# Performance work log

Hardware: AMD Instinct MI355X
Metric: run time of the kernel (lower is better)

## Reference

```python
import jax, jax.numpy as jnp
import numpy as np

NEG_INF = -1.0e9


def setup_inputs() -> dict:
    key = jax.random.key(0)
    ks = jax.random.split(key, 7)
    B, D, L, N, K = 4096, 512, 20, 8192, 64
    return {
        "inputs_embed": jax.random.normal(ks[0], (B, D), jnp.float32),
        "labels_embed": jax.random.normal(ks[1], (B, D), jnp.float32),
        "labels": jax.random.normal(ks[2], (B, L), jnp.float32),
        "all_labels_embed": jax.random.normal(ks[3], (N, D), jnp.float32),
        "all_labels": jax.random.normal(ks[4], (N, L), jnp.float32),
        "neg_ids_in": jax.random.randint(ks[5], (B, K), 0, B, jnp.int32),
        "neg_ids_lb": jax.random.randint(ks[6], (B, K), 0, N, jnp.int32),
    }


def reference(inputs_embed, labels_embed, labels, all_labels_embed, all_labels,
              neg_ids_in, neg_ids_lb):
    # --- negative sampling (indices supplied; equals tf.gather of tiled table) ---
    neg_ie = inputs_embed[neg_ids_in]        # [B,K,D] negatives from inputs
    neg_le = all_labels_embed[neg_ids_lb]    # [B,K,D] negatives from label table
    # bad-negative masks: negative label features identical to the positive's
    bad_in = jnp.all(labels[neg_ids_in] == labels[:, None, :], axis=-1).astype(inputs_embed.dtype)      # [B,K]
    bad_lb = jnp.all(all_labels[neg_ids_lb] == labels[:, None, :], axis=-1).astype(inputs_embed.dtype)  # [B,K]

    # --- similarities (dot products) ---
    sim_pos = jnp.sum(inputs_embed * labels_embed, axis=-1, keepdims=True)            # [B,1]
    sim_neg_il = jnp.einsum("bd,bkd->bk", inputs_embed, neg_le) + NEG_INF * bad_lb    # [B,K]
    sim_neg_ll = jnp.einsum("bd,bkd->bk", labels_embed, neg_le) + NEG_INF * bad_lb
    sim_neg_ii = jnp.einsum("bd,bkd->bk", inputs_embed, neg_ie) + NEG_INF * bad_in
    sim_neg_li = jnp.einsum("bd,bkd->bk", labels_embed, neg_ie) + NEG_INF * bad_in

    # --- accuracy ---
    max_all = jnp.max(jnp.concatenate([sim_pos, sim_neg_il], axis=-1), axis=-1)
    acc = jnp.mean((max_all == sim_pos[:, 0]).astype(jnp.float32))

    # --- softmax loss, correct class at index 0 ---
    logits = jnp.concatenate([sim_pos, sim_neg_il, sim_neg_ll, sim_neg_ii, sim_neg_li], axis=-1)  # [B,1+4K]
    per_ex = -jax.nn.log_softmax(logits, axis=-1)[:, 0]   # [B]

    # --- confidence-based loss scaling: loss_scale(-per_ex) ---
    q = jnp.exp(-per_ex)
    scale = jnp.where(jnp.max(q) > 0.5,
                      jax.lax.stop_gradient(((1.0 - q) / 0.5) ** 4),
                      jnp.ones_like(q))
    loss = jnp.mean(per_ex * scale)
    return loss, acc
```

## Files before the change

kernel.cpp:

```cpp
#include <hip/hip_runtime.h>
#include <hip/hip_bf16.h>

#define BB 4096
#define DD 512
#define LLAB 20
#define NN 8192
#define KK 64

constexpr float kNegInf = -1.0e9f;
constexpr float kLn2 = 0.69314718055994530942f;
constexpr float kWlPe = 2.5f;
constexpr float kWlTie = 2.0f;

#define OFF_STATS 16384
#define OFF_SP    16640
#define OFF_SIE   33024
#define OFF_SLE   49408
#define OFF_SALE  65792
#define OFF_HLAB  98560
#define OFF_HAL   131328
#define OFF_IEQ   196864
#define OFF_LEQ   2294016
#define OFF_ALEQ  4391168
#define WS_NEED   (OFF_ALEQ + (size_t)NN * DD)

__device__ __forceinline__ float dot4(const float4& a, const float4& b) {
  return a.x * b.x + a.y * b.y + a.z * b.z + a.w * b.w;
}

__device__ __forceinline__ float waveReduceSum(float v) {
#pragma unroll
  for (int s = 1; s < 64; s <<= 1) v += __shfl_xor(v, s);
  return v;
}

__device__ __forceinline__ float waveReduceMax(float v) {
#pragma unroll
  for (int s = 1; s < 64; s <<= 1) v = fmaxf(v, __shfl_xor(v, s));
  return v;
}

__device__ __forceinline__ float waveReduceMin(float v) {
#pragma unroll
  for (int s = 1; s < 64; s <<= 1) v = fminf(v, __shfl_xor(v, s));
  return v;
}

__device__ __forceinline__ unsigned long long hash20(const float* __restrict__ p) {
  unsigned long long h = 1469598103934665603ull;
#pragma unroll
  for (int t = 0; t < LLAB; ++t) {
    h ^= (unsigned long long)__float_as_uint(p[t]);
    h *= 1099511628211ull;
  }
  return h;
}

__device__ __forceinline__ int sdot4i(unsigned a, unsigned b, int acc) {
#if __has_builtin(__builtin_amdgcn_sdot4)
  return __builtin_amdgcn_sdot4((int)a, (int)b, acc, false);
#else
#pragma unroll
  for (int t = 0; t < 4; ++t)
    acc += (int)(signed char)(a >> (8 * t)) * (int)(signed char)(b >> (8 * t));
  return acc;
#endif
}

__device__ __forceinline__ unsigned pk4i8(float a, float b, float c, float d, float inv) {
  const int q0 = (int)rintf(a * inv);
  const int q1 = (int)rintf(b * inv);
  const int q2 = (int)rintf(c * inv);
  const int q3 = (int)rintf(d * inv);
  return (q0 & 255) | ((q1 & 255) << 8) | ((q2 & 255) << 16) | ((q3 & 255) << 24);
}

__device__ __forceinline__ float max8abs(const float4& a, const float4& c) {
  return fmaxf(fmaxf(fmaxf(fabsf(a.x), fabsf(a.y)), fmaxf(fabsf(a.z), fabsf(a.w))),
               fmaxf(fmaxf(fabsf(c.x), fabsf(c.y)), fmaxf(fabsf(c.z), fabsf(c.w))));
}

__global__ void init_kernel(unsigned* stats) {
  if (threadIdx.x == 0) stats[0] = 0u;
}

__global__ __launch_bounds__(256) void prep_kernel(
    const float* __restrict__ ie, const float* __restrict__ le,
    const float* __restrict__ ale, const float* __restrict__ labels,
    const float* __restrict__ al, char* __restrict__ ie_q,
    char* __restrict__ le_q, char* __restrict__ ale_q,
    float* __restrict__ s_ie, float* __restrict__ s_le,
    float* __restrict__ s_ale, float* __restrict__ sp,
    unsigned long long* __restrict__ h_lab,
    unsigned long long* __restrict__ h_al, unsigned* __restrict__ stats) {
  const int tid = threadIdx.x;
  const int lane = tid & 63;
  const int wave = tid >> 6;
  const int w = blockIdx.x * 4 + wave;

  if (w < BB) {
    const float4* i4 = (const float4*)(ie + (size_t)w * DD);
    const float4* l4 = (const float4*)(le + (size_t)w * DD);
    const float4 a0 = i4[2 * lane], a1 = i4[2 * lane + 1];
    const float4 b0 = l4[2 * lane], b1 = l4[2 * lane + 1];
    float p = dot4(a0, b0) + dot4(a1, b1);
    p = waveReduceSum(p);
    float mi = fmaxf(waveReduceMax(max8abs(a0, a1)), 1e-20f);
    const float inv_i = 127.0f / mi;
    uint2 oi;
    oi.x = pk4i8(a0.x, a0.y, a0.z, a0.w, inv_i);
    oi.y = pk4i8(a1.x, a1.y, a1.z, a1.w, inv_i);
    ((uint2*)(ie_q + (size_t)w * DD))[lane] = oi;
    float ml = fmaxf(waveReduceMax(max8abs(b0, b1)), 1e-20f);
    const float inv_l = 127.0f / ml;
    uint2 ol;
    ol.x = pk4i8(b0.x, b0.y, b0.z, b0.w, inv_l);
    ol.y = pk4i8(b1.x, b1.y, b1.z, b1.w, inv_l);
    ((uint2*)(le_q + (size_t)w * DD))[lane] = ol;
    if (lane == 0) {
      sp[w] = p;
      s_ie[w] = mi * (1.0f / 127.0f);
      s_le[w] = ml * (1.0f / 127.0f);
    }
  } else {
    const int row = w - BB;
    const float4* r4 = (const float4*)(ale + (size_t)row * DD);
    const float4 a = r4[2 * lane], c = r4[2 * lane + 1];
    float mx = fmaxf(waveReduceMax(max8abs(a, c)), 1e-20f);
    const float inv = 127.0f / mx;
    uint2 o;
    o.x = pk4i8(a.x, a.y, a.z, a.w, inv);
    o.y = pk4i8(c.x, c.y, c.z, c.w, inv);
    ((uint2*)(ale_q + (size_t)row * DD))[lane] = o;
    if (lane == 0) s_ale[row] = mx * (1.0f / 127.0f);
  }

  const int g = blockIdx.x * 256 + tid;
  if (g == 0) stats[0] = 0u;
  if (g < BB) h_lab[g] = hash20(labels + (size_t)g * LLAB);
  else if (g < BB + NN) h_al[g - BB] = hash20(al + (size_t)(g - BB) * LLAB);
}

__device__ __forceinline__ void row_f32_body(
    int b, const float* __restrict__ ie, const float* __restrict__ le,
    const float* __restrict__ labels, const float* __restrict__ ale,
    const float* __restrict__ al, const int* __restrict__ nin,
    const int* __restrict__ nlb, float* __restrict__ per_ex,
    unsigned* __restrict__ stats, bool count_acc, float* sims, float* wred) {
  const int tid = threadIdx.x;
  const int lane = tid & 63;
  const int wave = tid >> 6;

  const float4* ie4 = (const float4*)(ie + (size_t)b * DD);
  const float4* le4 = (const float4*)(le + (size_t)b * DD);
  float4 ier0 = ie4[lane], ier1 = ie4[lane + 64];
  float4 ler0 = le4[lane], ler1 = le4[lane + 64];
  float lab = (lane < LLAB) ? labels[(size_t)b * LLAB + lane] : 0.0f;

  if (wave == 0) {
    float p = dot4(ier0, ler0) + dot4(ier1, ler1);
    p = waveReduceSum(p);
    if (lane == 0) sims[0] = p;
  }

#pragma unroll 2
  for (int kk = 0; kk < KK / 4; ++kk) {
    const int k = wave * (KK / 4) + kk;
    const int j_lb = __builtin_amdgcn_readfirstlane(nlb[(size_t)b * KK + k]);
    const int j_in = __builtin_amdgcn_readfirstlane(nin[(size_t)b * KK + k]);

    const float4* rle = (const float4*)(ale + (size_t)j_lb * DD);
    const float4* rie = (const float4*)(ie + (size_t)j_in * DD);
    float4 vle0 = rle[lane], vle1 = rle[lane + 64];
    float4 vie0 = rie[lane], vie1 = rie[lane + 64];

    bool ein = true, elb = true;
    if (lane < LLAB) {
      ein = (labels[(size_t)j_in * LLAB + lane] == lab);
      elb = (al[(size_t)j_lb * LLAB + lane] == lab);
    }
    const bool bad_in = (__ballot(ein) == ~0ull);
    const bool bad_lb = (__ballot(elb) == ~0ull);

    float a_il = dot4(vle0, ier0) + dot4(vle1, ier1);
    float a_ll = dot4(vle0, ler0) + dot4(vle1, ler1);
    float a_ii = dot4(vie0, ier0) + dot4(vie1, ier1);
    float a_li = dot4(vie0, ler0) + dot4(vie1, ler1);

    const bool oddl = (lane & 1) != 0;
    float sx = oddl ? a_il : a_ii;
    float sy = oddl ? a_ll : a_li;
    float rx = __shfl_xor(sx, 1);
    float ry = __shfl_xor(sy, 1);
    float mx = (oddl ? a_ii : a_il) + rx;
    float my = (oddl ? a_li : a_ll) + ry;
    const bool hi2 = (lane & 2) != 0;
    float s1 = hi2 ? mx : my;
    float r1 = __shfl_xor(s1, 2);
    float v = (hi2 ? my : mx) + r1;
    v += __shfl_xor(v, 4);
    v += __shfl_xor(v, 8);
    v += __shfl_xor(v, 16);
    v += __shfl_xor(v, 32);

    if (lane < 4) {
      const bool badf = (lane & 1) ? bad_in : bad_lb;
      const float s = badf ? v + kNegInf : v;
      const int slot = ((lane & 1) << 1) | ((lane >> 1) & 1);
      sims[1 + slot * KK + k] = s;
    }
  }
  __syncthreads();

  const float v = sims[1 + tid];
  const float s0 = sims[0];
  float wmax = waveReduceMax(v);
  if (lane == 0) wred[wave] = wmax;
  __syncthreads();
  float m = fmaxf(fmaxf(wred[0], wred[1]), fmaxf(wred[2], wred[3]));
  m = fmaxf(m, s0);
  const float e = expf(v - m);
  float wsum = waveReduceSum(e);
  if (lane == 0) wred[4 + wave] = wsum;
  __syncthreads();
  if (tid == 0) {
    const float tot = wred[4] + wred[5] + wred[6] + wred[7] + expf(s0 - m);
    per_ex[b] = m + logf(tot) - s0;
    if (count_acc) {
      const float max_il = wred[0];
      if (s0 >= max_il) atomicAdd(&stats[0], 1u);
    }
  }
}

__global__ __launch_bounds__(256, 4) void row_i8_kernel(
    const float* __restrict__ ie, const float* __restrict__ le,
    const float* __restrict__ labels, const float* __restrict__ ale,
    const float* __restrict__ al, const char* __restrict__ ie_q,
    const char* __restrict__ le_q, const char* __restrict__ ale_q,
    const float* __restrict__ s_ie, const float* __restrict__ s_le,
    const float* __restrict__ s_ale, const float* __restrict__ sp,
    const unsigned long long* __restrict__ h_lab,
    const unsigned long long* __restrict__ h_al,
    const int* __restrict__ nin, const int* __restrict__ nlb,
    float* __restrict__ per_ex, unsigned* __restrict__ stats) {
  const int b = blockIdx.x;
  const int tid = threadIdx.x;
  const int lane = tid & 63;
  const int wave = tid >> 6;
  const int c = lane & 3;
  const int g = lane >> 2;

  __shared__ uint4 qls4[64];
  __shared__ float simsX[1 + 4 * KK];
  __shared__ float wred[12];
  __shared__ int do_fix;

  const int wuni = __builtin_amdgcn_readfirstlane(wave);
  const int k = wuni * 16 + g;

  const int jl = nlb[b * KK + k];
  const int ji = nin[b * KK + k];
  const unsigned long long hb = h_lab[b];
  const bool bad_lb = (h_al[jl] == hb);
  const bool bad_in = (h_lab[ji] == hb);
  const float sA = s_ale[jl];
  const float sB = s_ie[ji];

  const uint4* arow = (const uint4*)(ale_q + (size_t)jl * DD);
  const uint4* brow = (const uint4*)(ie_q + (size_t)ji * DD);
  uint4 Ar[8], Br[8];
#pragma unroll
  for (int i = 0; i < 8; ++i) {
    Ar[i] = arow[i * 4 + c];
    Br[i] = brow[i * 4 + c];
  }

  if (wave == 0) {
    if (lane < 32) qls4[lane] = ((const uint4*)(ie_q + (size_t)b * DD))[lane];
    else qls4[lane] = ((const uint4*)(le_q + (size_t)b * DD))[lane - 32];
  }
  __syncthreads();

  int il = 0, ll = 0, ii = 0, li = 0;
#pragma unroll
  for (int i = 0; i < 8; ++i) {
    const uint4 qi = qls4[i * 4 + c];
    const uint4 ql = qls4[32 + i * 4 + c];
    il = sdot4i(Ar[i].x, qi.x, il); il = sdot4i(Ar[i].y, qi.y, il);
    il = sdot4i(Ar[i].z, qi.z, il); il = sdot4i(Ar[i].w, qi.w, il);
    ll = sdot4i(Ar[i].x, ql.x, ll); ll = sdot4i(Ar[i].y, ql.y, ll);
    ll = sdot4i(Ar[i].z, ql.z, ll); ll = sdot4i(Ar[i].w, ql.w, ll);
    ii = sdot4i(Br[i].x, qi.x, ii); ii = sdot4i(Br[i].y, qi.y, ii);
    ii = sdot4i(Br[i].z, qi.z, ii); ii = sdot4i(Br[i].w, qi.w, ii);
    li = sdot4i(Br[i].x, ql.x, li); li = sdot4i(Br[i].y, ql.y, li);
    li = sdot4i(Br[i].z, ql.z, li); li = sdot4i(Br[i].w, ql.w, li);
  }

  const bool odd = (lane & 1) != 0;
  const int x = odd ? il : ii;
  const int y = odd ? ll : li;
  const int rx = __shfl_xor(x, 1);
  const int ry = __shfl_xor(y, 1);
  const int aa = (odd ? ii : il) + rx;
  const int bb2 = (odd ? li : ll) + ry;
  const bool hi2 = (lane & 2) != 0;
  const int s1 = hi2 ? aa : bb2;
  const int r1 = __shfl_xor(s1, 2);
  const int vi = (hi2 ? bb2 : aa) + r1;

  const float srow = (c & 1) ? sB : sA;
  const float sq = (c & 2) ? s_le[b] : s_ie[b];
  const float v = (float)vi * (srow * sq);
  const bool badf = (c & 1) ? bad_in : bad_lb;
  const float s = badf ? v + kNegInf : v;

  const float s0 = sp[b];

  float m_w = waveReduceMax(s);
  float mil_w = waveReduceMax((c == 0) ? s : -3.0e38f);
  if (lane == 0) {
    wred[wave] = m_w;
    wred[4 + wave] = mil_w;
  }
  __syncthreads();
  float m = fmaxf(fmaxf(fmaxf(wred[0], wred[1]), fmaxf(wred[2], wred[3])), s0);
  const float e = expf(s - m);
  float sum_w = waveReduceSum(e);
  if (lane == 0) wred[8 + wave] = sum_w;
  __syncthreads();
  if (tid == 0) {
    const float tot = wred[8] + wred[9] + wred[10] + wred[11] + expf(s0 - m);
    const float pe = m + logf(tot) - s0;
    per_ex[b] = pe;
    const float max_il = fmaxf(fmaxf(wred[4], wred[5]), fmaxf(wred[6], wred[7]));
    const bool wl_row = (pe < kWlPe) || (fabsf(s0 - max_il) < kWlTie);
    do_fix = wl_row ? 1 : 0;
    if (!wl_row && s0 >= max_il) atomicAdd(&stats[0], 1u);
  }
  __syncthreads();

  if (do_fix) {
    row_f32_body(b, ie, le, labels, ale, al, nin, nlb, per_ex, stats,
                 true, simsX, wred);
  }
}

__global__ __launch_bounds__(256) void row_f32_kernel(
    const float* __restrict__ ie, const float* __restrict__ le,
    const float* __restrict__ labels, const float* __restrict__ ale,
    const float* __restrict__ al, const int* __restrict__ nin,
    const int* __restrict__ nlb, float* __restrict__ per_ex,
    unsigned* __restrict__ stats) {
  __shared__ float sims[1 + 4 * KK];
  __shared__ float wred[8];
  row_f32_body(blockIdx.x, ie, le, labels, ale, al, nin, nlb, per_ex, stats,
               true, sims, wred);
}

__global__ __launch_bounds__(256) void finalize_kernel(
    const float* __restrict__ per_ex, const unsigned* __restrict__ stats,
    float* __restrict__ out) {
  __shared__ float pe_s[BB];
  __shared__ float wred[8];
  const int tid = threadIdx.x;
  const int lane = tid & 63;
  const int wave = tid >> 6;

  float mn = 1.0e30f;
#pragma unroll 4
  for (int i = tid; i < BB; i += 256) {
    const float v = per_ex[i];
    pe_s[i] = v;
    mn = fminf(mn, v);
  }
  mn = waveReduceMin(mn);
  if (lane == 0) wred[wave] = mn;
  __syncthreads();
  const float minpe = fminf(fminf(wred[0], wred[1]), fminf(wred[2], wred[3]));
  const bool scale_on = (minpe < kLn2);
  __syncthreads();

  float sum = 0.0f;
#pragma unroll 4
  for (int i = tid; i < BB; i += 256) {
    const float pe = pe_s[i];
    float s = 1.0f;
    if (scale_on) {
      const float q = expf(-pe);
      const float t = 2.0f * (1.0f - q);
      const float t2 = t * t;
      s = t2 * t2;
    }
    sum += pe * s;
  }
  sum = waveReduceSum(sum);
  if (lane == 0) wred[4 + wave] = sum;
  __syncthreads();
  if (tid == 0) {
    const float tot = wred[4] + wred[5] + wred[6] + wred[7];
    out[0] = tot / (float)BB;
    out[1] = (float)stats[0] / (float)BB;
  }
}

extern "C" void kernel_launch(void* const* d_in, const int* in_sizes, int n_in,
                              void* d_out, int out_size, void* d_ws, size_t ws_size,
                              hipStream_t stream) {
  const float* ie = (const float*)d_in[0];
  const float* le = (const float*)d_in[1];
  const float* labels = (const float*)d_in[2];
  const float* ale = (const float*)d_in[3];
  const float* al = (const float*)d_in[4];
  const int* nin = (const int*)d_in[5];
  const int* nlb = (const int*)d_in[6];
  float* out = (float*)d_out;

  float* per_ex = (float*)d_ws;
  unsigned* stats = (unsigned*)((char*)d_ws + OFF_STATS);

  if (ws_size >= WS_NEED) {
    char* ie_q = (char*)d_ws + OFF_IEQ;
    char* le_q = (char*)d_ws + OFF_LEQ;
    char* ale_q = (char*)d_ws + OFF_ALEQ;
    float* s_ie = (float*)((char*)d_ws + OFF_SIE);
    float* s_le = (float*)((char*)d_ws + OFF_SLE);
    float* s_ale = (float*)((char*)d_ws + OFF_SALE);
    float* sp = (float*)((char*)d_ws + OFF_SP);
    unsigned long long* h_lab = (unsigned long long*)((char*)d_ws + OFF_HLAB);
    unsigned long long* h_al = (unsigned long long*)((char*)d_ws + OFF_HAL);
    const int prep_blocks = (BB + NN) / 4;
    hipLaunchKernelGGL(prep_kernel, dim3(prep_blocks), dim3(256), 0, stream,
                       ie, le, ale, labels, al, ie_q, le_q, ale_q,
                       s_ie, s_le, s_ale, sp, h_lab, h_al, stats);
    hipLaunchKernelGGL(row_i8_kernel, dim3(BB), dim3(256), 0, stream,
                       ie, le, labels, ale, al, ie_q, le_q, ale_q,
                       s_ie, s_le, s_ale, sp, h_lab, h_al, nin, nlb,
                       per_ex, stats);
  } else {
    hipLaunchKernelGGL(init_kernel, dim3(1), dim3(64), 0, stream, stats);
    hipLaunchKernelGGL(row_f32_kernel, dim3(BB), dim3(256), 0, stream,
                       ie, le, labels, ale, al, nin, nlb, per_ex, stats);
  }
  hipLaunchKernelGGL(finalize_kernel, dim3(1), dim3(256), 0, stream,
                     per_ex, stats, out);
}
```

Measured before the change: 53.29 us.

## Move f32 fixup rows to worklist kernel and reduce loss via fixed-point atomics

The int8 row kernel now runs 512 threads with 8 lanes per negative and no longer does an inline f32 recompute. Rows that are near-tie or low-loss are pushed to a worklist and recomputed by a separate persistent fixup kernel. Each row's loss, scaled loss and the running minimum are accumulated into banked fixed-point atomics, so the final reduction only reads 64 banks instead of all per-example values. This removes per-block divergence from inline fixups and shrinks the finalize pass, at the cost of one extra launch, atomic traffic, and precision that depends on the fixed-point encoding and the int8 tie heuristics.

```diff
diff --git a/kernel.cpp b/kernel.cpp
--- a/kernel.cpp
+++ b/kernel.cpp
@@ -11,17 +11,23 @@
 constexpr float kLn2 = 0.69314718055994530942f;
 constexpr float kWlPe = 2.5f;
 constexpr float kWlTie = 2.0f;
-
+constexpr double kFix = 1073741824.0;
+
+#define OFF_PEREX 0
 #define OFF_STATS 16384
-#define OFF_SP    16640
-#define OFF_SIE   33024
-#define OFF_SLE   49408
-#define OFF_SALE  65792
-#define OFF_HLAB  98560
-#define OFF_HAL   131328
-#define OFF_IEQ   196864
-#define OFF_LEQ   2294016
-#define OFF_ALEQ  4391168
+#define OFF_MINPE (16384 + 256)
+#define OFF_SUMP  (16384 + 512)
+#define OFF_SUMS  (16384 + 1024)
+#define OFF_WL    20480
+#define OFF_SP    36864
+#define OFF_SIE   53248
+#define OFF_SLE   69632
+#define OFF_SALE  86016
+#define OFF_HLAB  118784
+#define OFF_HAL   151552
+#define OFF_IEQ   217088
+#define OFF_LEQ   (OFF_IEQ + (size_t)BB * DD)
+#define OFF_ALEQ  (OFF_LEQ + (size_t)BB * DD)
 #define WS_NEED   (OFF_ALEQ + (size_t)NN * DD)
 
 __device__ __forceinline__ float dot4(const float4& a, const float4& b) {
@@ -78,6 +84,24 @@
 __device__ __forceinline__ float max8abs(const float4& a, const float4& c) {
   return fmaxf(fmaxf(fmaxf(fabsf(a.x), fabsf(a.y)), fmaxf(fabsf(a.z), fabsf(a.w))),
                fmaxf(fmaxf(fabsf(c.x), fabsf(c.y)), fmaxf(fabsf(c.z), fabsf(c.w))));
+}
+
+__device__ __forceinline__ float loss_scale(float pe) {
+  const float q = expf(-pe);
+  const float t = 2.0f * (1.0f - q);
+  const float t2 = t * t;
+  return t2 * t2;
+}
+
+__device__ __forceinline__ void accum_loss(int b, float pe, unsigned* minpeB,
+                                           unsigned long long* sumP,
+                                           unsigned long long* sumS) {
+  const float pc = fmaxf(pe, 0.0f);
+  const int bank = b & 63;
+  atomicMin(&minpeB[bank], __float_as_uint(pc));
+  atomicAdd(&sumP[bank], (unsigned long long)((double)pc * kFix + 0.5));
+  atomicAdd(&sumS[bank],
+            (unsigned long long)((double)(pc * loss_scale(pc)) * kFix + 0.5));
 }
 
 __global__ void init_kernel(unsigned* stats) {
@@ -92,7 +116,9 @@
     float* __restrict__ s_ie, float* __restrict__ s_le,
     float* __restrict__ s_ale, float* __restrict__ sp,
     unsigned long long* __restrict__ h_lab,
-    unsigned long long* __restrict__ h_al, unsigned* __restrict__ stats) {
+    unsigned long long* __restrict__ h_al, unsigned* __restrict__ stats,
+    unsigned* __restrict__ minpeB, unsigned long long* __restrict__ sumP,
+    unsigned long long* __restrict__ sumS) {
   const int tid = threadIdx.x;
   const int lane = tid & 63;
   const int wave = tid >> 6;
@@ -136,9 +162,140 @@
   }
 
   const int g = blockIdx.x * 256 + tid;
-  if (g == 0) stats[0] = 0u;
+  if (g < 2) stats[g] = 0u;
+  if (g < 64) {
+    minpeB[g] = 0x7F800000u;
+    sumP[g] = 0ull;
+    sumS[g] = 0ull;
+  }
   if (g < BB) h_lab[g] = hash20(labels + (size_t)g * LLAB);
   else if (g < BB + NN) h_al[g - BB] = hash20(al + (size_t)(g - BB) * LLAB);
+}
+
+__global__ __launch_bounds__(512, 8) void row_i8_kernel(
+    const char* __restrict__ ie_q, const char* __restrict__ le_q,
+    const char* __restrict__ ale_q, const float* __restrict__ s_ie,
+    const float* __restrict__ s_le, const float* __restrict__ s_ale,
+    const float* __restrict__ sp, const unsigned long long* __restrict__ h_lab,
+    const unsigned long long* __restrict__ h_al,
+    const int* __restrict__ nin, const int* __restrict__ nlb,
+    int* __restrict__ wl, unsigned* __restrict__ stats,
+    unsigned* __restrict__ minpeB, unsigned long long* __restrict__ sumP,
+    unsigned long long* __restrict__ sumS) {
+  const int b = blockIdx.x;
+  const int tid = threadIdx.x;
+  const int lane = tid & 63;
+  const int wave = tid >> 6;
+  const int o = lane & 7;
+  const int oct = lane >> 3;
+
+  __shared__ uint4 qls4[64];
+  __shared__ float wredm[8], wreds[8];
+  __shared__ int iflags[8];
+
+  const int k = wave * 8 + oct;
+  const int jl = nlb[b * KK + k];
+  const int ji = nin[b * KK + k];
+
+  const uint4* arow = (const uint4*)(ale_q + (size_t)jl * DD);
+  const uint4* brow = (const uint4*)(ie_q + (size_t)ji * DD);
+  uint4 Ar[4], Br[4];
+#pragma unroll
+  for (int j = 0; j < 4; ++j) {
+    Ar[j] = arow[o + 8 * j];
+    Br[j] = brow[o + 8 * j];
+  }
+
+  const unsigned long long hb = h_lab[b];
+  const bool bad_lb = (h_al[jl] == hb);
+  const bool bad_in = (h_lab[ji] == hb);
+  const float sA = s_ale[jl];
+  const float sB = s_ie[ji];
+  const float s0 = sp[b];
+
+  if (wave == 0) {
+    if (lane < 32) qls4[lane] = ((const uint4*)(ie_q + (size_t)b * DD))[lane];
+    else qls4[lane] = ((const uint4*)(le_q + (size_t)b * DD))[lane - 32];
+  }
+  __syncthreads();
+
+  int il = 0, ll = 0, ii = 0, li = 0;
+#pragma unroll
+  for (int j = 0; j < 4; ++j) {
+    const uint4 qi = qls4[o + 8 * j];
+    const uint4 ql = qls4[32 + o + 8 * j];
+    il = sdot4i(Ar[j].x, qi.x, il); il = sdot4i(Ar[j].y, qi.y, il);
+    il = sdot4i(Ar[j].z, qi.z, il); il = sdot4i(Ar[j].w, qi.w, il);
+    ll = sdot4i(Ar[j].x, ql.x, ll); ll = sdot4i(Ar[j].y, ql.y, ll);
+    ll = sdot4i(Ar[j].z, ql.z, ll); ll = sdot4i(Ar[j].w, ql.w, ll);
+    ii = sdot4i(Br[j].x, qi.x, ii); ii = sdot4i(Br[j].y, qi.y, ii);
+    ii = sdot4i(Br[j].z, qi.z, ii); ii = sdot4i(Br[j].w, qi.w, ii);
+    li = sdot4i(Br[j].x, ql.x, li); li = sdot4i(Br[j].y, ql.y, li);
+    li = sdot4i(Br[j].z, ql.z, li); li = sdot4i(Br[j].w, ql.w, li);
+  }
+
+  const bool odd = (lane & 1) != 0;
+  const int x = odd ? il : ii;
+  const int y = odd ? ll : li;
+  const int rx = __shfl_xor(x, 1);
+  const int ry = __shfl_xor(y, 1);
+  const int aa = (odd ? ii : il) + rx;
+  const int bb2 = (odd ? li : ll) + ry;
+  const bool hi2 = (lane & 2) != 0;
+  const int s1 = hi2 ? aa : bb2;
+  const int r1 = __shfl_xor(s1, 2);
+  int vi = (hi2 ? bb2 : aa) + r1;
+  vi += __shfl_xor(vi, 4);
+
+  const int c = lane & 3;
+  const bool real = (lane & 4) == 0;
+  const float srow = (c & 1) ? sB : sA;
+  const float sq = (c & 2) ? s_le[b] : s_ie[b];
+  const float v = (float)vi * (srow * sq);
+  const bool badf = (c & 1) ? bad_in : bad_lb;
+  const float s = badf ? v + kNegInf : v;
+
+  const bool is_il = (c == 0) && real;
+  const bool okA = !is_il || (s <= s0);
+  const bool exB = is_il && (s > s0 - kWlTie);
+  const bool albB = !is_il || (s < s0 + kWlTie);
+  const int flags = ((__ballot(okA) == ~0ull) ? 1 : 0) |
+                    ((__ballot(exB) != 0ull) ? 2 : 0) |
+                    ((__ballot(albB) == ~0ull) ? 4 : 0);
+
+  float m_w = waveReduceMax(s);
+  if (lane == 0) {
+    wredm[wave] = m_w;
+    iflags[wave] = flags;
+  }
+  __syncthreads();
+  float m = s0;
+#pragma unroll
+  for (int t = 0; t < 8; ++t) m = fmaxf(m, wredm[t]);
+  const float e = real ? expf(s - m) : 0.0f;
+  float sum_w = waveReduceSum(e);
+  if (lane == 0) wreds[wave] = sum_w;
+  __syncthreads();
+  if (tid == 0) {
+    float tot = expf(s0 - m);
+    int allok = 1, anyex = 0, allb = 1;
+#pragma unroll
+    for (int t = 0; t < 8; ++t) {
+      tot += wreds[t];
+      allok &= (iflags[t] & 1);
+      anyex |= (iflags[t] & 2);
+      allb &= (iflags[t] >> 2) & 1;
+    }
+    const float pe = m + logf(tot) - s0;
+    const bool band = (anyex != 0) && (allb != 0);
+    if ((pe < kWlPe) || band) {
+      const unsigned p = atomicAdd(&stats[1], 1u);
+      wl[p] = b;
+    } else {
+      if (allok) atomicAdd(&stats[0], 1u);
+      accum_loss(b, pe, minpeB, sumP, sumS);
+    }
+  }
 }
 
 __device__ __forceinline__ void row_f32_body(
@@ -233,119 +390,6 @@
   }
 }
 
-__global__ __launch_bounds__(256, 4) void row_i8_kernel(
-    const float* __restrict__ ie, const float* __restrict__ le,
-    const float* __restrict__ labels, const float* __restrict__ ale,
-    const float* __restrict__ al, const char* __restrict__ ie_q,
-    const char* __restrict__ le_q, const char* __restrict__ ale_q,
-    const float* __restrict__ s_ie, const float* __restrict__ s_le,
-    const float* __restrict__ s_ale, const float* __restrict__ sp,
-    const unsigned long long* __restrict__ h_lab,
-    const unsigned long long* __restrict__ h_al,
-    const int* __restrict__ nin, const int* __restrict__ nlb,
-    float* __restrict__ per_ex, unsigned* __restrict__ stats) {
-  const int b = blockIdx.x;
-  const int tid = threadIdx.x;
-  const int lane = tid & 63;
-  const int wave = tid >> 6;
-  const int c = lane & 3;
-  const int g = lane >> 2;
-
-  __shared__ uint4 qls4[64];
-  __shared__ float simsX[1 + 4 * KK];
-  __shared__ float wred[12];
-  __shared__ int do_fix;
-
-  const int wuni = __builtin_amdgcn_readfirstlane(wave);
-  const int k = wuni * 16 + g;
-
-  const int jl = nlb[b * KK + k];
-  const int ji = nin[b * KK + k];
-  const unsigned long long hb = h_lab[b];
-  const bool bad_lb = (h_al[jl] == hb);
-  const bool bad_in = (h_lab[ji] == hb);
-  const float sA = s_ale[jl];
-  const float sB = s_ie[ji];
-
-  const uint4* arow = (const uint4*)(ale_q + (size_t)jl * DD);
-  const uint4* brow = (const uint4*)(ie_q + (size_t)ji * DD);
-  uint4 Ar[8], Br[8];
-#pragma unroll
-  for (int i = 0; i < 8; ++i) {
-    Ar[i] = arow[i * 4 + c];
-    Br[i] = brow[i * 4 + c];
-  }
-
-  if (wave == 0) {
-    if (lane < 32) qls4[lane] = ((const uint4*)(ie_q + (size_t)b * DD))[lane];
-    else qls4[lane] = ((const uint4*)(le_q + (size_t)b * DD))[lane - 32];
-  }
-  __syncthreads();
-
-  int il = 0, ll = 0, ii = 0, li = 0;
-#pragma unroll
-  for (int i = 0; i < 8; ++i) {
-    const uint4 qi = qls4[i * 4 + c];
-    const uint4 ql = qls4[32 + i * 4 + c];
-    il = sdot4i(Ar[i].x, qi.x, il); il = sdot4i(Ar[i].y, qi.y, il);
-    il = sdot4i(Ar[i].z, qi.z, il); il = sdot4i(Ar[i].w, qi.w, il);
-    ll = sdot4i(Ar[i].x, ql.x, ll); ll = sdot4i(Ar[i].y, ql.y, ll);
-    ll = sdot4i(Ar[i].z, ql.z, ll); ll = sdot4i(Ar[i].w, ql.w, ll);
-    ii = sdot4i(Br[i].x, qi.x, ii); ii = sdot4i(Br[i].y, qi.y, ii);
-    ii = sdot4i(Br[i].z, qi.z, ii); ii = sdot4i(Br[i].w, qi.w, ii);
-    li = sdot4i(Br[i].x, ql.x, li); li = sdot4i(Br[i].y, ql.y, li);
-    li = sdot4i(Br[i].z, ql.z, li); li = sdot4i(Br[i].w, ql.w, li);
-  }
-
-  const bool odd = (lane & 1) != 0;
-  const int x = odd ? il : ii;
-  const int y = odd ? ll : li;
-  const int rx = __shfl_xor(x, 1);
-  const int ry = __shfl_xor(y, 1);
-  const int aa = (odd ? ii : il) + rx;
-  const int bb2 = (odd ? li : ll) + ry;
-  const bool hi2 = (lane & 2) != 0;
-  const int s1 = hi2 ? aa : bb2;
-  const int r1 = __shfl_xor(s1, 2);
-  const int vi = (hi2 ? bb2 : aa) + r1;
-
-  const float srow = (c & 1) ? sB : sA;
-  const float sq = (c & 2) ? s_le[b] : s_ie[b];
-  const float v = (float)vi * (srow * sq);
-  const bool badf = (c & 1) ? bad_in : bad_lb;
-  const float s = badf ? v + kNegInf : v;
-
-  const float s0 = sp[b];
-
-  float m_w = waveReduceMax(s);
-  float mil_w = waveReduceMax((c == 0) ? s : -3.0e38f);
-  if (lane == 0) {
-    wred[wave] = m_w;
-    wred[4 + wave] = mil_w;
-  }
-  __syncthreads();
-  float m = fmaxf(fmaxf(fmaxf(wred[0], wred[1]), fmaxf(wred[2], wred[3])), s0);
-  const float e = expf(s - m);
-  float sum_w = waveReduceSum(e);
-  if (lane == 0) wred[8 + wave] = sum_w;
-  __syncthreads();
-  if (tid == 0) {
-    const float tot = wred[8] + wred[9] + wred[10] + wred[11] + expf(s0 - m);
-    const float pe = m + logf(tot) - s0;
-    per_ex[b] = pe;
-    const float max_il = fmaxf(fmaxf(wred[4], wred[5]), fmaxf(wred[6], wred[7]));
-    const bool wl_row = (pe < kWlPe) || (fabsf(s0 - max_il) < kWlTie);
-    do_fix = wl_row ? 1 : 0;
-    if (!wl_row && s0 >= max_il) atomicAdd(&stats[0], 1u);
-  }
-  __syncthreads();
-
-  if (do_fix) {
-    row_f32_body(b, ie, le, labels, ale, al, nin, nlb, per_ex, stats,
-                 true, simsX, wred);
-  }
-}
-
 __global__ __launch_bounds__(256) void row_f32_kernel(
     const float* __restrict__ ie, const float* __restrict__ le,
     const float* __restrict__ labels, const float* __restrict__ ale,
@@ -358,6 +402,49 @@
                true, sims, wred);
 }
 
+__global__ __launch_bounds__(256) void fixup_kernel(
+    const float* __restrict__ ie, const float* __restrict__ le,
+    const float* __restrict__ labels, const float* __restrict__ ale,
+    const float* __restrict__ al, const int* __restrict__ nin,
+    const int* __restrict__ nlb, float* __restrict__ per_ex,
+    const int* __restrict__ wl, unsigned* __restrict__ stats,
+    unsigned* __restrict__ minpeB, unsigned long long* __restrict__ sumP,
+    unsigned long long* __restrict__ sumS) {
+  __shared__ float sims[1 + 4 * KK];
+  __shared__ float wred[8];
+  const int n = (int)stats[1];
+  for (int w = blockIdx.x; w < n; w += gridDim.x) {
+    const int b = wl[w];
+    row_f32_body(b, ie, le, labels, ale, al, nin, nlb, per_ex, stats,
+                 true, sims, wred);
+    if (threadIdx.x == 0) accum_loss(b, per_ex[b], minpeB, sumP, sumS);
+    __syncthreads();
+  }
+}
+
+__global__ __launch_bounds__(64) void finalize2_kernel(
+    const unsigned* __restrict__ stats, const unsigned* __restrict__ minpeB,
+    const unsigned long long* __restrict__ sumP,
+    const unsigned long long* __restrict__ sumS, float* __restrict__ out) {
+  const int lane = threadIdx.x;
+  unsigned mb = minpeB[lane];
+  unsigned long long p = sumP[lane];
+  unsigned long long q = sumS[lane];
+#pragma unroll
+  for (int s = 1; s < 64; s <<= 1) {
+    mb = min(mb, (unsigned)__shfl_xor((int)mb, s));
+    p += (unsigned long long)__shfl_xor((long long)p, s);
+    q += (unsigned long long)__shfl_xor((long long)q, s);
+  }
+  if (lane == 0) {
+    const float minpe = __uint_as_float(mb);
+    const bool scale_on = (minpe < kLn2);
+    const double tot = (double)(scale_on ? q : p) / kFix;
+    out[0] = (float)(tot / (double)BB);
+    out[1] = (float)stats[0] / (float)BB;
+  }
+}
+
 __global__ __launch_bounds__(256) void finalize_kernel(
     const float* __restrict__ per_ex, const unsigned* __restrict__ stats,
     float* __restrict__ out) {
@@ -385,14 +472,7 @@
 #pragma unroll 4
   for (int i = tid; i < BB; i += 256) {
     const float pe = pe_s[i];
-    float s = 1.0f;
-    if (scale_on) {
-      const float q = expf(-pe);
-      const float t = 2.0f * (1.0f - q);
-      const float t2 = t * t;
-      s = t2 * t2;
-    }
-    sum += pe * s;
+    sum += pe * (scale_on ? loss_scale(pe) : 1.0f);
   }
   sum = waveReduceSum(sum);
   if (lane == 0) wred[4 + wave] = sum;
@@ -429,19 +509,29 @@
     float* sp = (float*)((char*)d_ws + OFF_SP);
     unsigned long long* h_lab = (unsigned long long*)((char*)d_ws + OFF_HLAB);
     unsigned long long* h_al = (unsigned long long*)((char*)d_ws + OFF_HAL);
+    unsigned* minpeB = (unsigned*)((char*)d_ws + OFF_MINPE);
+    unsigned long long* sumP = (unsigned long long*)((char*)d_ws + OFF_SUMP);
+    unsigned long long* sumS = (unsigned long long*)((char*)d_ws + OFF_SUMS);
+    int* wl = (int*)((char*)d_ws + OFF_WL);
+
     const int prep_blocks = (BB + NN) / 4;
     hipLaunchKernelGGL(prep_kernel, dim3(prep_blocks), dim3(256), 0, stream,
                        ie, le, ale, labels, al, ie_q, le_q, ale_q,
-                       s_ie, s_le, s_ale, sp, h_lab, h_al, stats);
-    hipLaunchKernelGGL(row_i8_kernel, dim3(BB), dim3(256), 0, stream,
-                       ie, le, labels, ale, al, ie_q, le_q, ale_q,
-                       s_ie, s_le, s_ale, sp, h_lab, h_al, nin, nlb,
-                       per_ex, stats);
+                       s_ie, s_le, s_ale, sp, h_lab, h_al, stats,
+                       minpeB, sumP, sumS);
+    hipLaunchKernelGGL(row_i8_kernel, dim3(BB), dim3(512), 0, stream,
+                       ie_q, le_q, ale_q, s_ie, s_le, s_ale, sp, h_lab, h_al,
+                       nin, nlb, wl, stats, minpeB, sumP, sumS);
+    hipLaunchKernelGGL(fixup_kernel, dim3(128), dim3(256), 0, stream,
+                       ie, le, labels, ale, al, nin, nlb, per_ex, wl, stats,
+                       minpeB, sumP, sumS);
+    hipLaunchKernelGGL(finalize2_kernel, dim3(1), dim3(64), 0, stream,
+                       stats, minpeB, sumP, sumS, out);
   } else {
     hipLaunchKernelGGL(init_kernel, dim3(1), dim3(64), 0, stream, stats);
     hipLaunchKernelGGL(row_f32_kernel, dim3(BB), dim3(256), 0, stream,
                        ie, le, labels, ale, al, nin, nlb, per_ex, stats);
-  }
-  hipLaunchKernelGGL(finalize_kernel, dim3(1), dim3(256), 0, stream,
-                     per_ex, stats, out);
-}
+    hipLaunchKernelGGL(finalize_kernel, dim3(1), dim3(256), 0, stream,
+                       per_ex, stats, out);
+  }
+}
```

New measurement: 58.69 us. 1.1x slower.

## Fuse loss reduction into row kernel via banked fixed-point atomics, asm gather loads

Applied to the files above, without the earlier changes.

Each row's per-example loss, and its confidence-scaled variant, are accumulated into 64 banked fixed-point 64-bit atomic sums plus an atomic min. A tiny one-wave finalize kernel then picks the right sum, replacing the 4096-element finalize pass over per_ex. The row kernel also issues its int8 negative-row gathers with inline asm global_load_dwordx4 before the scalar lookups, and every wave stages the query vectors, so the block barrier before the dot products is dropped. This adds atomic traffic and fixed-point rounding, and clamps negative per-example losses to zero before accumulation.

```diff
diff --git a/kernel.cpp b/kernel.cpp
--- a/kernel.cpp
+++ b/kernel.cpp
@@ -11,18 +11,29 @@
 constexpr float kLn2 = 0.69314718055994530942f;
 constexpr float kWlPe = 2.5f;
 constexpr float kWlTie = 2.0f;
-
+constexpr double kFix = 1073741824.0;
+
+#define OFF_PEREX 0
 #define OFF_STATS 16384
-#define OFF_SP    16640
-#define OFF_SIE   33024
-#define OFF_SLE   49408
-#define OFF_SALE  65792
-#define OFF_HLAB  98560
-#define OFF_HAL   131328
-#define OFF_IEQ   196864
-#define OFF_LEQ   2294016
-#define OFF_ALEQ  4391168
+#define OFF_MINPE (16384 + 256)
+#define OFF_SUMP  (16384 + 512)
+#define OFF_SUMS  (16384 + 1024)
+#define OFF_SP    36864
+#define OFF_SIE   53248
+#define OFF_SLE   69632
+#define OFF_SALE  86016
+#define OFF_HLAB  118784
+#define OFF_HAL   151552
+#define OFF_IEQ   217088
+#define OFF_LEQ   (OFF_IEQ + (size_t)BB * DD)
+#define OFF_ALEQ  (OFF_LEQ + (size_t)BB * DD)
 #define WS_NEED   (OFF_ALEQ + (size_t)NN * DD)
+
+typedef unsigned u32x4 __attribute__((ext_vector_type(4)));
+
+#define GLD(dst, base, OFFSTR)                                        \
+  asm volatile("global_load_dwordx4 %0, %1, off offset:" OFFSTR      \
+               : "=v"(dst) : "v"(base) : "memory")
 
 __device__ __forceinline__ float dot4(const float4& a, const float4& b) {
   return a.x * b.x + a.y * b.y + a.z * b.z + a.w * b.w;
@@ -80,6 +91,24 @@
                fmaxf(fmaxf(fabsf(c.x), fabsf(c.y)), fmaxf(fabsf(c.z), fabsf(c.w))));
 }
 
+__device__ __forceinline__ float loss_scale(float pe) {
+  const float q = expf(-pe);
+  const float t = 2.0f * (1.0f - q);
+  const float t2 = t * t;
+  return t2 * t2;
+}
+
+__device__ __forceinline__ void accum_loss(int b, float pe, unsigned* minpeB,
+                                           unsigned long long* sumP,
+                                           unsigned long long* sumS) {
+  const float pc = fmaxf(pe, 0.0f);
+  const int bank = b & 63;
+  atomicMin(&minpeB[bank], __float_as_uint(pc));
+  atomicAdd(&sumP[bank], (unsigned long long)((double)pc * kFix + 0.5));
+  atomicAdd(&sumS[bank],
+            (unsigned long long)((double)(pc * loss_scale(pc)) * kFix + 0.5));
+}
+
 __global__ void init_kernel(unsigned* stats) {
   if (threadIdx.x == 0) stats[0] = 0u;
 }
@@ -92,7 +121,9 @@
     float* __restrict__ s_ie, float* __restrict__ s_le,
     float* __restrict__ s_ale, float* __restrict__ sp,
     unsigned long long* __restrict__ h_lab,
-    unsigned long long* __restrict__ h_al, unsigned* __restrict__ stats) {
+    unsigned long long* __restrict__ h_al, unsigned* __restrict__ stats,
+    unsigned* __restrict__ minpeB, unsigned long long* __restrict__ sumP,
+    unsigned long long* __restrict__ sumS) {
   const int tid = threadIdx.x;
   const int lane = tid & 63;
   const int wave = tid >> 6;
@@ -136,7 +167,12 @@
   }
 
   const int g = blockIdx.x * 256 + tid;
-  if (g == 0) stats[0] = 0u;
+  if (g < 2) stats[g] = 0u;
+  if (g < 64) {
+    minpeB[g] = 0x7F800000u;
+    sumP[g] = 0ull;
+    sumS[g] = 0ull;
+  }
   if (g < BB) h_lab[g] = hash20(labels + (size_t)g * LLAB);
   else if (g < BB + NN) h_al[g - BB] = hash20(al + (size_t)(g - BB) * LLAB);
 }
@@ -243,7 +279,9 @@
     const unsigned long long* __restrict__ h_lab,
     const unsigned long long* __restrict__ h_al,
     const int* __restrict__ nin, const int* __restrict__ nlb,
-    float* __restrict__ per_ex, unsigned* __restrict__ stats) {
+    float* __restrict__ per_ex, unsigned* __restrict__ stats,
+    unsigned* __restrict__ minpeB, unsigned long long* __restrict__ sumP,
+    unsigned long long* __restrict__ sumS) {
   const int b = blockIdx.x;
   const int tid = threadIdx.x;
   const int lane = tid & 63;
@@ -251,51 +289,61 @@
   const int c = lane & 3;
   const int g = lane >> 2;
 
-  __shared__ uint4 qls4[64];
+  __shared__ u32x4 qls4[64];
   __shared__ float simsX[1 + 4 * KK];
   __shared__ float wred[12];
   __shared__ int do_fix;
 
+  {
+    const u32x4* qsrc = (lane < 32)
+        ? ((const u32x4*)(ie_q + ((size_t)b << 9))) + lane
+        : ((const u32x4*)(le_q + ((size_t)b << 9))) + (lane - 32);
+    qls4[lane] = *qsrc;
+  }
+
   const int wuni = __builtin_amdgcn_readfirstlane(wave);
   const int k = wuni * 16 + g;
-
   const int jl = nlb[b * KK + k];
   const int ji = nin[b * KK + k];
+  const char* pa = ale_q + ((size_t)jl << 9) + (c << 4);
+  const char* pb = ie_q + ((size_t)ji << 9) + (c << 4);
+
+  u32x4 A0, A1, A2, A3, A4, A5, A6, A7;
+  u32x4 B0, B1, B2, B3, B4, B5, B6, B7;
+  GLD(A0, pa, "0");   GLD(A1, pa, "64");  GLD(A2, pa, "128"); GLD(A3, pa, "192");
+  GLD(A4, pa, "256"); GLD(A5, pa, "320"); GLD(A6, pa, "384"); GLD(A7, pa, "448");
+  GLD(B0, pb, "0");   GLD(B1, pb, "64");  GLD(B2, pb, "128"); GLD(B3, pb, "192");
+  GLD(B4, pb, "256"); GLD(B5, pb, "320"); GLD(B6, pb, "384"); GLD(B7, pb, "448");
+
   const unsigned long long hb = h_lab[b];
   const bool bad_lb = (h_al[jl] == hb);
   const bool bad_in = (h_lab[ji] == hb);
   const float sA = s_ale[jl];
   const float sB = s_ie[ji];
-
-  const uint4* arow = (const uint4*)(ale_q + (size_t)jl * DD);
-  const uint4* brow = (const uint4*)(ie_q + (size_t)ji * DD);
-  uint4 Ar[8], Br[8];
-#pragma unroll
-  for (int i = 0; i < 8; ++i) {
-    Ar[i] = arow[i * 4 + c];
-    Br[i] = brow[i * 4 + c];
-  }
-
-  if (wave == 0) {
-    if (lane < 32) qls4[lane] = ((const uint4*)(ie_q + (size_t)b * DD))[lane];
-    else qls4[lane] = ((const uint4*)(le_q + (size_t)b * DD))[lane - 32];
-  }
-  __syncthreads();
+  const float s0 = sp[b];
+  const float sqi = s_ie[b];
+  const float sql = s_le[b];
+
+  asm volatile("s_waitcnt vmcnt(0)" ::: "memory");
+  __builtin_amdgcn_sched_barrier(0);
 
   int il = 0, ll = 0, ii = 0, li = 0;
-#pragma unroll
-  for (int i = 0; i < 8; ++i) {
-    const uint4 qi = qls4[i * 4 + c];
-    const uint4 ql = qls4[32 + i * 4 + c];
-    il = sdot4i(Ar[i].x, qi.x, il); il = sdot4i(Ar[i].y, qi.y, il);
-    il = sdot4i(Ar[i].z, qi.z, il); il = sdot4i(Ar[i].w, qi.w, il);
-    ll = sdot4i(Ar[i].x, ql.x, ll); ll = sdot4i(Ar[i].y, ql.y, ll);
-    ll = sdot4i(Ar[i].z, ql.z, ll); ll = sdot4i(Ar[i].w, ql.w, ll);
-    ii = sdot4i(Br[i].x, qi.x, ii); ii = sdot4i(Br[i].y, qi.y, ii);
-    ii = sdot4i(Br[i].z, qi.z, ii); ii = sdot4i(Br[i].w, qi.w, ii);
-    li = sdot4i(Br[i].x, ql.x, li); li = sdot4i(Br[i].y, ql.y, li);
-    li = sdot4i(Br[i].z, ql.z, li); li = sdot4i(Br[i].w, ql.w, li);
-  }
+#define STEP(Ai, Bi, i)                                              \
+  {                                                                  \
+    const u32x4 qi = qls4[(i) * 4 + c];                              \
+    const u32x4 ql = qls4[32 + (i) * 4 + c];                         \
+    il = sdot4i(Ai.x, qi.x, il); il = sdot4i(Ai.y, qi.y, il);        \
+    il = sdot4i(Ai.z, qi.z, il); il = sdot4i(Ai.w, qi.w, il);        \
+    ll = sdot4i(Ai.x, ql.x, ll); ll = sdot4i(Ai.y, ql.y, ll);        \
+    ll = sdot4i(Ai.z, ql.z, ll); ll = sdot4i(Ai.w, ql.w, ll);        \
+    ii = sdot4i(Bi.x, qi.x, ii); ii = sdot4i(Bi.y, qi.y, ii);        \
+    ii = sdot4i(Bi.z, qi.z, ii); ii = sdot4i(Bi.w, qi.w, ii);        \
+    li = sdot4i(Bi.x, ql.x, li); li = sdot4i(Bi.y, ql.y, li);        \
+    li = sdot4i(Bi.z, ql.z, li); li = sdot4i(Bi.w, ql.w, li);        \
+  }
+  STEP(A0, B0, 0) STEP(A1, B1, 1) STEP(A2, B2, 2) STEP(A3, B3, 3)
+  STEP(A4, B4, 4) STEP(A5, B5, 5) STEP(A6, B6, 6) STEP(A7, B7, 7)
+#undef STEP
 
   const bool odd = (lane & 1) != 0;
   const int x = odd ? il : ii;
@@ -310,12 +358,10 @@
   const int vi = (hi2 ? bb2 : aa) + r1;
 
   const float srow = (c & 1) ? sB : sA;
-  const float sq = (c & 2) ? s_le[b] : s_ie[b];
+  const float sq = (c & 2) ? sql : sqi;
   const float v = (float)vi * (srow * sq);
   const bool badf = (c & 1) ? bad_in : bad_lb;
   const float s = badf ? v + kNegInf : v;
-
-  const float s0 = sp[b];
 
   float m_w = waveReduceMax(s);
   float mil_w = waveReduceMax((c == 0) ? s : -3.0e38f);
@@ -330,19 +376,24 @@
   if (lane == 0) wred[8 + wave] = sum_w;
   __syncthreads();
   if (tid == 0) {
-    const float tot = wred[8] + wred[9] + wred[10] + wred[11] + expf(s0 - m);
+    const float tot =
+        wred[8] + wred[9] + wred[10] + wred[11] + expf(s0 - m);
     const float pe = m + logf(tot) - s0;
     per_ex[b] = pe;
     const float max_il = fmaxf(fmaxf(wred[4], wred[5]), fmaxf(wred[6], wred[7]));
     const bool wl_row = (pe < kWlPe) || (fabsf(s0 - max_il) < kWlTie);
     do_fix = wl_row ? 1 : 0;
-    if (!wl_row && s0 >= max_il) atomicAdd(&stats[0], 1u);
+    if (!wl_row) {
+      if (s0 >= max_il) atomicAdd(&stats[0], 1u);
+      accum_loss(b, pe, minpeB, sumP, sumS);
+    }
   }
   __syncthreads();
 
   if (do_fix) {
     row_f32_body(b, ie, le, labels, ale, al, nin, nlb, per_ex, stats,
                  true, simsX, wred);
+    if (tid == 0) accum_loss(b, per_ex[b], minpeB, sumP, sumS);
   }
 }
 
@@ -358,6 +409,29 @@
                true, sims, wred);
 }
 
+__global__ __launch_bounds__(64) void finalize2_kernel(
+    const unsigned* __restrict__ stats, const unsigned* __restrict__ minpeB,
+    const unsigned long long* __restrict__ sumP,
+    const unsigned long long* __restrict__ sumS, float* __restrict__ out) {
+  const int lane = threadIdx.x;
+  unsigned mb = minpeB[lane];
+  unsigned long long p = sumP[lane];
+  unsigned long long q = sumS[lane];
+#pragma unroll
+  for (int s = 1; s < 64; s <<= 1) {
+    mb = min(mb, (unsigned)__shfl_xor((int)mb, s));
+    p += (unsigned long long)__shfl_xor((long long)p, s);
+    q += (unsigned long long)__shfl_xor((long long)q, s);
+  }
+  if (lane == 0) {
+    const float minpe = __uint_as_float(mb);
+    const bool scale_on = (minpe < kLn2);
+    const double tot = (double)(scale_on ? q : p) / kFix;
+    out[0] = (float)(tot / (double)BB);
+    out[1] = (float)stats[0] / (float)BB;
+  }
+}
+
 __global__ __launch_bounds__(256) void finalize_kernel(
     const float* __restrict__ per_ex, const unsigned* __restrict__ stats,
     float* __restrict__ out) {
@@ -385,14 +459,7 @@
 #pragma unroll 4
   for (int i = tid; i < BB; i += 256) {
     const float pe = pe_s[i];
-    float s = 1.0f;
-    if (scale_on) {
-      const float q = expf(-pe);
-      const float t = 2.0f * (1.0f - q);
-      const float t2 = t * t;
-      s = t2 * t2;
-    }
-    sum += pe * s;
+    sum += pe * (scale_on ? loss_scale(pe) : 1.0f);
   }
   sum = waveReduceSum(sum);
   if (lane == 0) wred[4 + wave] = sum;
@@ -429,19 +496,26 @@
     float* sp = (float*)((char*)d_ws + OFF_SP);
     unsigned long long* h_lab = (unsigned long long*)((char*)d_ws + OFF_HLAB);
     unsigned long long* h_al = (unsigned long long*)((char*)d_ws + OFF_HAL);
+    unsigned* minpeB = (unsigned*)((char*)d_ws + OFF_MINPE);
+    unsigned long long* sumP = (unsigned long long*)((char*)d_ws + OFF_SUMP);
+    unsigned long long* sumS = (unsigned long long*)((char*)d_ws + OFF_SUMS);
+
     const int prep_blocks = (BB + NN) / 4;
     hipLaunchKernelGGL(prep_kernel, dim3(prep_blocks), dim3(256), 0, stream,
                        ie, le, ale, labels, al, ie_q, le_q, ale_q,
-                       s_ie, s_le, s_ale, sp, h_lab, h_al, stats);
+                       s_ie, s_le, s_ale, sp, h_lab, h_al, stats,
+                       minpeB, sumP, sumS);
     hipLaunchKernelGGL(row_i8_kernel, dim3(BB), dim3(256), 0, stream,
                        ie, le, labels, ale, al, ie_q, le_q, ale_q,
                        s_ie, s_le, s_ale, sp, h_lab, h_al, nin, nlb,
-                       per_ex, stats);
+                       per_ex, stats, minpeB, sumP, sumS);
+    hipLaunchKernelGGL(finalize2_kernel, dim3(1), dim3(64), 0, stream,
+                       stats, minpeB, sumP, sumS, out);
   } else {
     hipLaunchKernelGGL(init_kernel, dim3(1), dim3(64), 0, stream, stats);
     hipLaunchKernelGGL(row_f32_kernel, dim3(BB), dim3(256), 0, stream,
                        ie, le, labels, ale, al, nin, nlb, per_ex, stats);
-  }
-  hipLaunchKernelGGL(finalize_kernel, dim3(1), dim3(256), 0, stream,
-                     per_ex, stats, out);
-}
+    hipLaunchKernelGGL(finalize_kernel, dim3(1), dim3(256), 0, stream,
+                       per_ex, stats, out);
+  }
+}
```

Result: no change. 53.63 us (+0.6%).
